# Kernel tuning notes

Measured on AMD Instinct MI355X. Metric: run time of the kernel, lower is better.

The kernel has to match this reference:

```python
import jax, jax.numpy as jnp
import numpy as np

B, SQ, SV, DQ, DV, U = 16, 128, 128, 512, 512, 256


def setup_inputs() -> dict:
    key = jax.random.key(0)
    ks = jax.random.split(key, 8)
    scale = 0.02
    return {
        "query": jax.random.normal(ks[0], (B, SQ, DQ), dtype=jnp.float32),
        "values": jax.random.normal(ks[1], (B, SV, DV), dtype=jnp.float32),
        "W1": jax.random.normal(ks[2], (DQ, U), dtype=jnp.float32) * scale,
        "b1": jnp.zeros((U,), dtype=jnp.float32),
        "W2": jax.random.normal(ks[3], (DV, U), dtype=jnp.float32) * scale,
        "b2": jnp.zeros((U,), dtype=jnp.float32),
        "Vw": jax.random.normal(ks[4], (U,), dtype=jnp.float32) * scale,
        "Vb": jnp.zeros((1,), dtype=jnp.float32),
    }


def reference(query, values, W1, b1, W2, b2, Vw, Vb):
    # query: [B,Sq,Dq], values: [B,Sv,Dv]  (3D branch of the Keras layer)
    s1 = jnp.einsum("bqd,du->bqu", query, W1) + b1   # [B,Sq,U]
    s2 = jnp.einsum("bvd,du->bvu", values, W2) + b2  # [B,Sv,U]
    # broadcast add -> tanh -> V projection (the large fused intermediate)
    t = jnp.tanh(s1[:, :, None, :] + s2[:, None, :, :])  # [B,Sq,Sv,U]
    score = jnp.einsum("bqvu,u->bqv", t, Vw) + Vb[0]     # [B,Sq,Sv]
    attention_weights = jax.nn.softmax(score, axis=2)    # softmax over Sv (axis=2)
    context_vector = jnp.einsum("bqv,bvd->bqd", attention_weights, values)  # [B,Sq,Dv]
    # original returns weights with trailing singleton dim from Dense(1)
    return context_vector, attention_weights[..., None]
```

## Files before the change

### kernel.cpp

```cpp
#include <hip/hip_runtime.h>

#define B_  16
#define SQ_ 128
#define SV_ 128
#define DQ_ 512
#define DV_ 512
#define U_  256

typedef float f32x4 __attribute__((ext_vector_type(4)));
typedef short s16x4 __attribute__((ext_vector_type(4)));

__device__ __forceinline__ short f2bf(float f) {
  unsigned u = __float_as_uint(f);
  u += 0x7fffu + ((u >> 16) & 1u);
  return (short)(u >> 16);
}

__global__ __launch_bounds__(256) void k_proj(
    const float* __restrict__ Q, const float* __restrict__ Vv,
    const float* __restrict__ W1, const float* __restrict__ b1,
    const float* __restrict__ W2, const float* __restrict__ b2,
    float* __restrict__ E1, float* __restrict__ E2)
{
  const int which = blockIdx.z;
  const float* __restrict__ X    = which ? Vv : Q;
  const float* __restrict__ W    = which ? W2 : W1;
  const float* __restrict__ bias = which ? b2 : b1;
  float* __restrict__ E          = which ? E2 : E1;

  const int lane  = threadIdx.x & 63;
  const int wid   = threadIdx.x >> 6;
  const int row16 = lane & 15;
  const int quad  = lane >> 4;

  const int m0 = blockIdx.x * 64 + (wid >> 1) * 32;
  const int n0 = blockIdx.y * 32 + (wid & 1) * 16;

  f32x4 acc[2];
  acc[0] = (f32x4){0.f,0.f,0.f,0.f};
  acc[1] = (f32x4){0.f,0.f,0.f,0.f};

  for (int k0 = 0; k0 < DQ_; k0 += 16) {
    s16x4 af[2], bfr;
    #pragma unroll
    for (int mt = 0; mt < 2; ++mt) {
      f32x4 av = *(const f32x4*)&X[(m0 + mt * 16 + row16) * DQ_ + k0 + quad * 4];
      af[mt][0] = f2bf(av[0]); af[mt][1] = f2bf(av[1]);
      af[mt][2] = f2bf(av[2]); af[mt][3] = f2bf(av[3]);
    }
    #pragma unroll
    for (int j = 0; j < 4; ++j)
      bfr[j] = f2bf(W[(k0 + quad * 4 + j) * U_ + n0 + row16]);
    #pragma unroll
    for (int mt = 0; mt < 2; ++mt)
      acc[mt] = __builtin_amdgcn_mfma_f32_16x16x16bf16_1k(af[mt], bfr, acc[mt], 0, 0, 0);
  }

  float bv = bias[n0 + row16];
  #pragma unroll
  for (int mt = 0; mt < 2; ++mt)
    #pragma unroll
    for (int r = 0; r < 4; ++r) {
      float s = acc[mt][r] + bv;
      E[(m0 + mt * 16 + quad * 4 + r) * U_ + n0 + row16] = __expf(2.0f * s);
    }
}

__global__ __launch_bounds__(1024) void k_attn(
    const float* __restrict__ E1, const float* __restrict__ E2,
    const float* __restrict__ Vw, const float* __restrict__ values,
    float* __restrict__ out_ctx, float* __restrict__ out_w)
{
  __shared__ float e1s[8 * U_];
  __shared__ float vws[U_];
  __shared__ float part[4096];
  __shared__ float red[8];

  const int tid  = threadIdx.x;
  const int lane = tid & 63;
  const int wid  = tid >> 6;
  const int b  = blockIdx.y;
  const int q0 = blockIdx.x * 8;

  if (tid < 512) {
    int q = tid >> 6, u4 = tid & 63;
    ((f32x4*)e1s)[q * 64 + u4] =
        *(const f32x4*)&E1[(b * SQ_ + q0 + q) * U_ + u4 * 4];
  }
  if (tid < 256) vws[tid] = Vw[tid];
  __syncthreads();

  if (wid == 0) {
    float s = vws[lane] + vws[lane + 64] + vws[lane + 128] + vws[lane + 192];
    #pragma unroll
    for (int o = 32; o; o >>= 1) s += __shfl_xor(s, o);
    if (lane == 0) red[0] = s;
  }

  const int v5 = tid & 31;
  const int uh = (tid >> 5) & 7;
  const int vh = tid >> 8;
  const int v  = vh * 32 + v5;

  f32x4 e2r[8];
  {
    const f32x4* e2p = (const f32x4*)&E2[(b * SV_ + v) * U_ + uh * 32];
    #pragma unroll
    for (int uq = 0; uq < 8; ++uq) e2r[uq] = e2p[uq];
  }
  const f32x4* e1v = (const f32x4*)e1s;
  const f32x4* wv4 = (const f32x4*)vws;

  float acc[8];
  #pragma unroll
  for (int q = 0; q < 8; ++q) acc[q] = 0.f;

  #pragma unroll
  for (int uq = 0; uq < 8; ++uq) {
    f32x4 e2 = e2r[uq];
    f32x4 w  = wv4[uh * 8 + uq];
    #pragma unroll
    for (int q = 0; q < 8; ++q) {
      f32x4 e1 = e1v[q * 64 + uh * 8 + uq];
      float d0 = fmaf(e1[0], e2[0], 1.0f);
      float d1 = fmaf(e1[1], e2[1], 1.0f);
      float rp = __builtin_amdgcn_rcpf(d0 * d1);
      float n  = fmaf(w[1], d0, w[0] * d1);
      acc[q] = fmaf(rp, n, acc[q]);
      float d2 = fmaf(e1[2], e2[2], 1.0f);
      float d3 = fmaf(e1[3], e2[3], 1.0f);
      float rp2 = __builtin_amdgcn_rcpf(d2 * d3);
      float n2  = fmaf(w[3], d2, w[2] * d3);
      acc[q] = fmaf(rp2, n2, acc[q]);
    }
  }

  #pragma unroll
  for (int q = 0; q < 8; ++q) acc[q] += __shfl_xor(acc[q], 32);
  if (lane < 32) {
    int uhh = wid & 3;
    #pragma unroll
    for (int q = 0; q < 8; ++q) part[uhh * 1024 + q * 128 + v] = acc[q];
  }
  __syncthreads();

  {
    int q = tid >> 7, vv = tid & 127;
    float s = part[q * 128 + vv] + part[1024 + q * 128 + vv] +
              part[2048 + q * 128 + vv] + part[3072 + q * 128 + vv];
    part[q * 128 + vv] = red[0] - 2.0f * s;
  }
  __syncthreads();

  if (wid < 8) {
    int q = wid;
    float x0 = part[q * 128 + lane], x1 = part[q * 128 + lane + 64];
    float m = fmaxf(x0, x1);
    #pragma unroll
    for (int o = 32; o; o >>= 1) m = fmaxf(m, __shfl_xor(m, o));
    float e0 = __expf(x0 - m), e1 = __expf(x1 - m);
    float ssum = e0 + e1;
    #pragma unroll
    for (int o = 32; o; o >>= 1) ssum += __shfl_xor(ssum, o);
    float inv = __fdividef(1.0f, ssum);
    e0 *= inv; e1 *= inv;
    part[q * 128 + lane] = e0;
    part[q * 128 + lane + 64] = e1;
    int wbase = (b * SQ_ + q0 + q) * SV_;
    out_w[wbase + lane] = e0;
    out_w[wbase + lane + 64] = e1;
  }
  __syncthreads();

  const int d = tid & 511;
  const int h = tid >> 9;
  float c[8];
  #pragma unroll
  for (int q = 0; q < 8; ++q) c[q] = 0.f;
  const float* vb = values + (size_t)(b * SV_ + h * 64) * DV_ + d;
  for (int vl = 0; vl < 64; vl += 4) {
    f32x4 wq[8];
    #pragma unroll
    for (int q = 0; q < 8; ++q)
      wq[q] = *(const f32x4*)&part[q * 128 + h * 64 + vl];
    #pragma unroll
    for (int j = 0; j < 4; ++j) {
      float val = vb[(vl + j) * DV_];
      #pragma unroll
      for (int q = 0; q < 8; ++q) c[q] = fmaf(wq[q][j], val, c[q]);
    }
  }
  __syncthreads();
  if (h == 1) {
    #pragma unroll
    for (int q = 0; q < 8; ++q) part[q * 512 + d] = c[q];
  }
  __syncthreads();
  if (h == 0) {
    #pragma unroll
    for (int q = 0; q < 8; ++q)
      out_ctx[(b * SQ_ + q0 + q) * DV_ + d] = c[q] + part[q * 512 + d];
  }
}

extern "C" void kernel_launch(void* const* d_in, const int* in_sizes, int n_in,
                              void* d_out, int out_size, void* d_ws, size_t ws_size,
                              hipStream_t stream) {
  (void)in_sizes; (void)n_in; (void)out_size; (void)ws_size;
  const float* Q  = (const float*)d_in[0];
  const float* Vv = (const float*)d_in[1];
  const float* W1 = (const float*)d_in[2];
  const float* b1 = (const float*)d_in[3];
  const float* W2 = (const float*)d_in[4];
  const float* b2 = (const float*)d_in[5];
  const float* Vw = (const float*)d_in[6];

  float* out_ctx = (float*)d_out;
  float* out_w   = out_ctx + B_ * SQ_ * DV_;

  float* E1 = (float*)d_ws;
  float* E2 = E1 + 2048 * U_;

  k_proj<<<dim3(32, 8, 2), 256, 0, stream>>>(Q, Vv, W1, b1, W2, b2, E1, E2);
  k_attn<<<dim3(SQ_ / 8, B_), 1024, 0, stream>>>(E1, E2, Vw, Vv, out_ctx, out_w);
}
```

Baseline: 108.2 us.

## Pretranspose weights to bf16, pack conversions, merge reciprocals in tanh sum

Adds a prep kernel that transposes W1/W2 into bf16 K-contiguous layout so the projection kernel loads B fragments with one vector load instead of four strided scalar loads, and packs the A-operand bf16 conversion with a perm instruction. The attention inner loop now combines four terms over a single reciprocal instead of two, halving rcp count per u-quad. This costs an extra kernel launch and workspace, and multiplying four denominators risks overflow when the exp(2s) terms are large.

```diff
diff --git a/kernel.cpp b/kernel.cpp
--- a/kernel.cpp
+++ b/kernel.cpp
@@ -10,23 +10,56 @@
 typedef float f32x4 __attribute__((ext_vector_type(4)));
 typedef short s16x4 __attribute__((ext_vector_type(4)));
 
-__device__ __forceinline__ short f2bf(float f) {
-  unsigned u = __float_as_uint(f);
-  u += 0x7fffu + ((u >> 16) & 1u);
-  return (short)(u >> 16);
+__device__ __forceinline__ unsigned pk_bf16(float a, float b) {
+  unsigned ua = __float_as_uint(a); ua += 0x7fffu + ((ua >> 16) & 1u);
+  unsigned ub = __float_as_uint(b); ub += 0x7fffu + ((ub >> 16) & 1u);
+  return __builtin_amdgcn_perm(ub, ua, 0x07060302u);
+}
+
+__global__ __launch_bounds__(256) void k_prep(
+    const float* __restrict__ W1, const float* __restrict__ W2,
+    unsigned short* __restrict__ Wt1, unsigned short* __restrict__ Wt2)
+{
+  const float* __restrict__ W = blockIdx.z ? W2 : W1;
+  unsigned short* __restrict__ Wt = blockIdx.z ? Wt2 : Wt1;
+  __shared__ float tile[64][65];
+
+  const int t  = threadIdx.x;
+  const int k0 = blockIdx.x * 64, n0 = blockIdx.y * 64;
+  const int r  = t >> 4, c4 = (t & 15) * 4;
+
+  #pragma unroll
+  for (int p = 0; p < 4; ++p) {
+    f32x4 v = *(const f32x4*)&W[(k0 + p * 16 + r) * U_ + n0 + c4];
+    tile[p * 16 + r][c4]     = v[0];
+    tile[p * 16 + r][c4 + 1] = v[1];
+    tile[p * 16 + r][c4 + 2] = v[2];
+    tile[p * 16 + r][c4 + 3] = v[3];
+  }
+  __syncthreads();
+  #pragma unroll
+  for (int p = 0; p < 4; ++p) {
+    int rr = p * 16 + r;
+    float v0 = tile[c4][rr], v1 = tile[c4 + 1][rr];
+    float v2 = tile[c4 + 2][rr], v3 = tile[c4 + 3][rr];
+    uint2 o;
+    o.x = pk_bf16(v0, v1);
+    o.y = pk_bf16(v2, v3);
+    *(uint2*)&Wt[(n0 + rr) * DQ_ + k0 + c4] = o;
+  }
 }
 
 __global__ __launch_bounds__(256) void k_proj(
     const float* __restrict__ Q, const float* __restrict__ Vv,
-    const float* __restrict__ W1, const float* __restrict__ b1,
-    const float* __restrict__ W2, const float* __restrict__ b2,
+    const unsigned short* __restrict__ Wt1, const float* __restrict__ b1,
+    const unsigned short* __restrict__ Wt2, const float* __restrict__ b2,
     float* __restrict__ E1, float* __restrict__ E2)
 {
   const int which = blockIdx.z;
-  const float* __restrict__ X    = which ? Vv : Q;
-  const float* __restrict__ W    = which ? W2 : W1;
+  const float* __restrict__ X = which ? Vv : Q;
+  const unsigned short* __restrict__ Wt = which ? Wt2 : Wt1;
   const float* __restrict__ bias = which ? b2 : b1;
-  float* __restrict__ E          = which ? E2 : E1;
+  float* __restrict__ E = which ? E2 : E1;
 
   const int lane  = threadIdx.x & 63;
   const int wid   = threadIdx.x >> 6;
@@ -36,34 +69,33 @@
   const int m0 = blockIdx.x * 64 + (wid >> 1) * 32;
   const int n0 = blockIdx.y * 32 + (wid & 1) * 16;
 
-  f32x4 acc[2];
-  acc[0] = (f32x4){0.f,0.f,0.f,0.f};
-  acc[1] = (f32x4){0.f,0.f,0.f,0.f};
-
-  for (int k0 = 0; k0 < DQ_; k0 += 16) {
-    s16x4 af[2], bfr;
-    #pragma unroll
-    for (int mt = 0; mt < 2; ++mt) {
-      f32x4 av = *(const f32x4*)&X[(m0 + mt * 16 + row16) * DQ_ + k0 + quad * 4];
-      af[mt][0] = f2bf(av[0]); af[mt][1] = f2bf(av[1]);
-      af[mt][2] = f2bf(av[2]); af[mt][3] = f2bf(av[3]);
-    }
-    #pragma unroll
-    for (int j = 0; j < 4; ++j)
-      bfr[j] = f2bf(W[(k0 + quad * 4 + j) * U_ + n0 + row16]);
-    #pragma unroll
-    for (int mt = 0; mt < 2; ++mt)
-      acc[mt] = __builtin_amdgcn_mfma_f32_16x16x16bf16_1k(af[mt], bfr, acc[mt], 0, 0, 0);
-  }
-
-  float bv = bias[n0 + row16];
-  #pragma unroll
-  for (int mt = 0; mt < 2; ++mt)
-    #pragma unroll
-    for (int r = 0; r < 4; ++r) {
-      float s = acc[mt][r] + bv;
-      E[(m0 + mt * 16 + quad * 4 + r) * U_ + n0 + row16] = __expf(2.0f * s);
-    }
+  const float* a0 = X + (size_t)(m0 + row16) * DQ_ + quad * 4;
+  const float* a1 = a0 + 16 * DQ_;
+  const unsigned short* bp = Wt + (size_t)(n0 + row16) * DQ_ + quad * 4;
+
+  f32x4 acc0 = (f32x4){0.f, 0.f, 0.f, 0.f};
+  f32x4 acc1 = (f32x4){0.f, 0.f, 0.f, 0.f};
+
+  for (int k = 0; k < DQ_; k += 16) {
+    f32x4 av0 = *(const f32x4*)(a0 + k);
+    f32x4 av1 = *(const f32x4*)(a1 + k);
+    uint2 bu  = *(const uint2*)(bp + k);
+    uint2 u0, u1;
+    u0.x = pk_bf16(av0[0], av0[1]); u0.y = pk_bf16(av0[2], av0[3]);
+    u1.x = pk_bf16(av1[0], av1[1]); u1.y = pk_bf16(av1[2], av1[3]);
+    s16x4 A0 = *(s16x4*)&u0;
+    s16x4 A1 = *(s16x4*)&u1;
+    s16x4 Bf = *(s16x4*)&bu;
+    acc0 = __builtin_amdgcn_mfma_f32_16x16x16bf16_1k(A0, Bf, acc0, 0, 0, 0);
+    acc1 = __builtin_amdgcn_mfma_f32_16x16x16bf16_1k(A1, Bf, acc1, 0, 0, 0);
+  }
+
+  const float bv = bias[n0 + row16];
+  #pragma unroll
+  for (int r = 0; r < 4; ++r) {
+    E[(size_t)(m0 + quad * 4 + r) * U_ + n0 + row16]      = __expf(2.f * (acc0[r] + bv));
+    E[(size_t)(m0 + 16 + quad * 4 + r) * U_ + n0 + row16] = __expf(2.f * (acc1[r] + bv));
+  }
 }
 
 __global__ __launch_bounds__(1024) void k_attn(
@@ -85,7 +117,7 @@
   if (tid < 512) {
     int q = tid >> 6, u4 = tid & 63;
     ((f32x4*)e1s)[q * 64 + u4] =
-        *(const f32x4*)&E1[(b * SQ_ + q0 + q) * U_ + u4 * 4];
+        *(const f32x4*)&E1[(size_t)(b * SQ_ + q0 + q) * U_ + u4 * 4];
   }
   if (tid < 256) vws[tid] = Vw[tid];
   __syncthreads();
@@ -104,7 +136,7 @@
 
   f32x4 e2r[8];
   {
-    const f32x4* e2p = (const f32x4*)&E2[(b * SV_ + v) * U_ + uh * 32];
+    const f32x4* e2p = (const f32x4*)&E2[(size_t)(b * SV_ + v) * U_ + uh * 32];
     #pragma unroll
     for (int uq = 0; uq < 8; ++uq) e2r[uq] = e2p[uq];
   }
@@ -122,16 +154,16 @@
     #pragma unroll
     for (int q = 0; q < 8; ++q) {
       f32x4 e1 = e1v[q * 64 + uh * 8 + uq];
-      float d0 = fmaf(e1[0], e2[0], 1.0f);
-      float d1 = fmaf(e1[1], e2[1], 1.0f);
-      float rp = __builtin_amdgcn_rcpf(d0 * d1);
-      float n  = fmaf(w[1], d0, w[0] * d1);
-      acc[q] = fmaf(rp, n, acc[q]);
-      float d2 = fmaf(e1[2], e2[2], 1.0f);
-      float d3 = fmaf(e1[3], e2[3], 1.0f);
-      float rp2 = __builtin_amdgcn_rcpf(d2 * d3);
-      float n2  = fmaf(w[3], d2, w[2] * d3);
-      acc[q] = fmaf(rp2, n2, acc[q]);
+      float d0 = fmaf(e1[0], e2[0], 1.f);
+      float d1 = fmaf(e1[1], e2[1], 1.f);
+      float d2 = fmaf(e1[2], e2[2], 1.f);
+      float d3 = fmaf(e1[3], e2[3], 1.f);
+      float p01 = d0 * d1, p23 = d2 * d3;
+      float n01 = fmaf(w[0], d1, w[1] * d0);
+      float n23 = fmaf(w[2], d3, w[3] * d2);
+      float num = fmaf(n01, p23, n23 * p01);
+      float rp  = __builtin_amdgcn_rcpf(p01 * p23);
+      acc[q] = fmaf(num, rp, acc[q]);
     }
   }
 
@@ -199,7 +231,7 @@
   if (h == 0) {
     #pragma unroll
     for (int q = 0; q < 8; ++q)
-      out_ctx[(b * SQ_ + q0 + q) * DV_ + d] = c[q] + part[q * 512 + d];
+      out_ctx[(size_t)(b * SQ_ + q0 + q) * DV_ + d] = c[q] + part[q * 512 + d];
   }
 }
 
@@ -220,7 +252,10 @@
 
   float* E1 = (float*)d_ws;
   float* E2 = E1 + 2048 * U_;
-
-  k_proj<<<dim3(32, 8, 2), 256, 0, stream>>>(Q, Vv, W1, b1, W2, b2, E1, E2);
+  unsigned short* Wt1 = (unsigned short*)(E2 + 2048 * U_);
+  unsigned short* Wt2 = Wt1 + U_ * DQ_;
+
+  k_prep<<<dim3(8, 4, 2), 256, 0, stream>>>(W1, W2, Wt1, Wt2);
+  k_proj<<<dim3(32, 8, 2), 256, 0, stream>>>(Q, Vv, Wt1, b1, Wt2, b2, E1, E2);
   k_attn<<<dim3(SQ_ / 8, B_), 1024, 0, stream>>>(E1, E2, Vw, Vv, out_ctx, out_w);
 }
```

Result: slower. 113.2 us (+4.7%).
